# Kernel tuning notes

Measured on AMD Instinct MI355X. Metric: run time of the kernel, lower is better.

The kernel has to match this reference:

```python
import jax, jax.numpy as jnp
import numpy as np

N = 50000        # num nodes
E = 800000       # num edges (before self loops)
IN = 256         # in_channels
H = 4            # heads
C = 32           # out_channels per head
NEG_SLOPE = 0.2


def _glorot(key, shape):
    fan = shape[-2] * (shape[-1] if len(shape) > 2 else 1) + shape[-1]
    # PyG glorot: uniform(-s, s) with s = sqrt(6 / (fan_in + fan_out))
    s = float(np.sqrt(6.0 / (shape[-2] + shape[-1])))
    return jax.random.uniform(key, shape, jnp.float32, -s, s)


def setup_inputs() -> dict:
    key = jax.random.key(0)
    k1, k2, k3, k4, k5 = jax.random.split(key, 5)
    x = jax.random.normal(k1, (N, IN), jnp.float32)
    src = jax.random.randint(k2, (E,), 0, N)
    dst = jax.random.randint(k3, (E,), 0, N)
    # guarantee no self loops (module removes them then re-adds exactly N loops)
    dst = jnp.where(dst == src, (dst + 1) % N, dst)
    edge_index = jnp.stack([src, dst]).astype(jnp.int32)
    weight = _glorot(k4, (IN, H * C))
    att = _glorot(k5, (1, H, 2 * C))
    bias = jnp.zeros((H * C,), jnp.float32)
    return {"x": x, "weight": weight, "att": att, "bias": bias,
            "edge_index": edge_index}


def reference(x, weight, att, bias, edge_index):
    n = x.shape[0]
    # linear projection -> [N, H, C]
    h = (x @ weight).reshape(n, H, C)
    # add self loops (input edge_index has none)
    loops = jnp.arange(n, dtype=edge_index.dtype)
    ei = jnp.concatenate([edge_index, jnp.stack([loops, loops])], axis=1)
    src, dst = ei[0], ei[1]          # flow source_to_target: j=src(row 0), i=dst(row 1)
    x_j = h[src]                     # [E', H, C] source features
    x_i = h[dst]                     # [E', H, C] target features
    wl = att[:, :, :C]               # applied to x_i (first half of concat)
    wr = att[:, :, C:]               # applied to x_j
    alpha = (x_i * wl).sum(-1) + (x_j * wr).sum(-1)   # [E', H]
    alpha = jax.nn.leaky_relu(alpha, NEG_SLOPE)
    # NOTE: module normalizes softmax over edge_index[0] (src) segments
    seg = src
    amax = jax.ops.segment_max(alpha, seg, num_segments=n)
    alpha = jnp.exp(alpha - amax[seg])
    denom = jax.ops.segment_sum(alpha, seg, num_segments=n)
    alpha = alpha / (denom[seg] + 1e-16)
    # weighted messages, aggregated at edge_index[i] = edge_index[1] (dst)
    msg = x_j * alpha[:, :, None]                     # [E', H, C]
    out = jax.ops.segment_sum(msg, dst, num_segments=n)  # [N, H, C]
    return out.reshape(n, H * C) + bias
```

## Files before the change

### kernel.cpp

```cpp
#include <hip/hip_runtime.h>
#include <hip/hip_fp16.h>
#include <math.h>


#define NH 4
#define CH 32
#define HC 128
#define IND 256
#define NEG_SLOPE 0.2f
#define CSH 8
#define NCB_MAX 256
#define CHUNK 4096
#define BCAP 6144

typedef __attribute__((ext_vector_type(8))) short bf16x8;
typedef __attribute__((ext_vector_type(16))) float f32x16;

__device__ __forceinline__ unsigned short f2bf(float f) {
    unsigned int u = __float_as_uint(f);
    unsigned int r = (u + 0x7FFFu + ((u >> 16) & 1u)) >> 16;
    return (unsigned short)r;
}
__device__ __forceinline__ float bf2f(unsigned short s) {
    return __uint_as_float(((unsigned int)s) << 16);
}

__global__ __launch_bounds__(256) void k_wprep(const float* __restrict__ W,
                                               unsigned short* __restrict__ WT_bf,
                                               int* __restrict__ gcurS,
                                               int* __restrict__ gcurD) {
    int t = blockIdx.x * 256 + threadIdx.x;
    if (blockIdx.x == 0) { gcurS[threadIdx.x] = 0; gcurD[threadIdx.x] = 0; }
    if (t < IND * HC) {
        int c = t >> 8;
        int k = t & 255;
        WT_bf[t] = f2bf(W[k * HC + c]);
    }
}

__global__ __launch_bounds__(512) void k_gs(const float* __restrict__ x,
                                            const unsigned short* __restrict__ WT_bf,
                                            const float* __restrict__ att,
                                            unsigned short* __restrict__ h_bf,
                                            float* __restrict__ al,
                                            float* __restrict__ ar,
                                            const int* __restrict__ ei,
                                            int* __restrict__ gcurS,
                                            int* __restrict__ gcurD,
                                            unsigned int* __restrict__ recS,
                                            unsigned int* __restrict__ recD,
                                            int E, int NE, int ncb, int ngb, int N) {
    __shared__ __align__(16) unsigned short smem[67840];

    const int tid = threadIdx.x;

    if (blockIdx.x >= ngb) {
        unsigned int* srt = (unsigned int*)smem;
        int* cnt  = (int*)(srt + CHUNK);
        int* off  = cnt + NCB_MAX;
        int* cur  = off + NCB_MAX;
        int* gpos = cur + NCB_MAX;
        int* sc   = gpos + NCB_MAX;

        const int t0 = (blockIdx.x - ngb) * CHUNK;
        const int m  = min(CHUNK, NE - t0);

        unsigned int myrec[CHUNK / 512];
        int nmy = 0;
        for (int i = tid; i < m; i += 512) {
            int t = t0 + i;
            int src, dst;
            if (t < E) { src = ei[t]; dst = ei[E + t]; }
            else       { src = dst = t - E; }
            myrec[nmy++] = (unsigned int)src | ((unsigned int)dst << 16);
        }

        for (int side = 0; side < 2; side++) {
            if (tid < 256) cnt[tid] = 0;
            __syncthreads();
            int mybkt[CHUNK / 512];
            for (int k = 0; k < nmy; k++) {
                unsigned int r = myrec[k];
                int node = side ? (int)(r >> 16) : (int)(r & 0xFFFFu);
                mybkt[k] = node >> CSH;
                atomicAdd(&cnt[mybkt[k]], 1);
            }
            __syncthreads();
            int v = (tid < 256) ? cnt[tid] : 0;
            if (tid < 256) sc[tid] = v;
            __syncthreads();
            for (int o = 1; o < 256; o <<= 1) {
                int t = (tid >= o && tid < 256) ? sc[tid - o] : 0;
                __syncthreads();
                if (tid < 256) sc[tid] += t;
                __syncthreads();
            }
            if (tid < 256) { off[tid] = sc[tid] - v; cur[tid] = sc[tid] - v; }
            __syncthreads();
            for (int k = 0; k < nmy; k++) {
                int p = atomicAdd(&cur[mybkt[k]], 1);
                srt[p] = myrec[k];
            }
            __syncthreads();
            int* gcur = side ? gcurD : gcurS;
            if (tid < ncb) {
                int c = cnt[tid];
                gpos[tid] = c ? atomicAdd(&gcur[tid], c) : 0;
            }
            __syncthreads();
            unsigned int* recX = side ? recD : recS;
            for (int i = tid; i < m; i += 512) {
                unsigned int r = srt[i];
                int node = side ? (int)(r >> 16) : (int)(r & 0xFFFFu);
                int cb = node >> CSH;
                int p  = gpos[cb] + (i - off[cb]);
                if (p < BCAP)
                    recX[(size_t)cb * BCAP + p] = r;
            }
            __syncthreads();
        }
        return;
    }

    unsigned short* xs0 = smem;
    unsigned short* xs1 = smem + 17408;
    unsigned short* wsT = smem + 34816;

    const int row0 = blockIdx.x * 256;
    const int wave = tid >> 6;
    const int lane = tid & 63;
    const int n32  = lane & 31;
    const int half = lane >> 5;

    {
        int c  = tid >> 2;
        int kq = (tid & 3) * 64;
        const unsigned short* src = WT_bf + c * IND + kq;
        unsigned short* dst = wsT + c * 258 + kq;
#pragma unroll
        for (int j = 0; j < 64; j += 8)
            *(int4*)(dst + j) = *(const int4*)(src + j);
    }

    float4 v[8];
#define STAGE_LOAD(p)                                                        \
    {                                                                        \
        _Pragma("unroll")                                                    \
        for (int j = 0; j < 8; j++) {                                        \
            int fid = j * 512 + tid;                                         \
            int gr  = row0 + (fid >> 4);                                     \
            float4 t = make_float4(0.f, 0.f, 0.f, 0.f);                      \
            if (gr < N)                                                      \
                t = *(const float4*)(x + (size_t)gr * IND + (p) * 64 +       \
                                     (fid & 15) * 4);                        \
            v[j] = t;                                                        \
        }                                                                    \
    }
#define STAGE_WRITE(buf)                                                     \
    {                                                                        \
        _Pragma("unroll")                                                    \
        for (int j = 0; j < 8; j++) {                                        \
            int fid = j * 512 + tid;                                         \
            int row = fid >> 4;                                              \
            ushort4 o;                                                       \
            o.x = f2bf(v[j].x); o.y = f2bf(v[j].y);                          \
            o.z = f2bf(v[j].z); o.w = f2bf(v[j].w);                          \
            *(ushort4*)((buf) + row * 68 + (fid & 15) * 4) = o;              \
        }                                                                    \
    }

    STAGE_LOAD(0);
    STAGE_WRITE(xs0);
    __syncthreads();

    f32x16 acc[4];
#pragma unroll
    for (int t = 0; t < 4; t++)
#pragma unroll
        for (int r = 0; r < 16; r++) acc[t][r] = 0.0f;

    const int arow = wave * 32 + n32;
#pragma unroll
    for (int p = 0; p < 4; p++) {
        if (p < 3) STAGE_LOAD(p + 1);
        const unsigned short* xb = (p & 1) ? xs1 : xs0;
#pragma unroll
        for (int s = 0; s < 4; s++) {
            bf16x8 a = *(const bf16x8*)(xb + arow * 68 + s * 16 + half * 8);
#pragma unroll
            for (int t = 0; t < 4; t++) {
                bf16x8 b = *(const bf16x8*)(wsT + (t * 32 + n32) * 258 +
                                            p * 64 + s * 16 + half * 8);
                acc[t] = __builtin_amdgcn_mfma_f32_32x32x16_bf16(a, b, acc[t], 0, 0, 0);
            }
        }
        if (p < 3) STAGE_WRITE((p & 1) ? xs0 : xs1);
        __syncthreads();
    }
#undef STAGE_LOAD
#undef STAGE_WRITE

    float* cs = (float*)smem;
    for (int pass = 0; pass < 2; pass++) {
        if ((wave >> 2) == pass) {
            const int lw = wave & 3;
#pragma unroll
            for (int t = 0; t < 4; t++)
#pragma unroll
                for (int r = 0; r < 16; r++) {
                    int rl = lw * 32 + (r & 3) + 8 * (r >> 2) + 4 * half;
                    cs[rl * 132 + t * 33 + n32] = acc[t][r];
                }
        }
        __syncthreads();

        const int rl   = tid >> 2;
        const int hq   = tid & 3;
        const int orow = row0 + pass * 128 + rl;
        if (orow < N) {
            const float* cr = cs + rl * 132 + hq * 33;
            unsigned short* hp = h_bf + (size_t)orow * HC + hq * CH;
#pragma unroll
            for (int c = 0; c < 32; c += 8) {
                ushort4 o0, o1;
                o0.x = f2bf(cr[c]);     o0.y = f2bf(cr[c + 1]);
                o0.z = f2bf(cr[c + 2]); o0.w = f2bf(cr[c + 3]);
                o1.x = f2bf(cr[c + 4]); o1.y = f2bf(cr[c + 5]);
                o1.z = f2bf(cr[c + 6]); o1.w = f2bf(cr[c + 7]);
                *(ushort4*)(hp + c) = o0;
                *(ushort4*)(hp + c + 4) = o1;
            }
            const float* w0 = att + hq * (2 * CH);
            float sl = 0.f, sr = 0.f;
#pragma unroll
            for (int c = 0; c < CH; c++) {
                float v2 = cr[c];
                sl += v2 * w0[c];
                sr += v2 * w0[CH + c];
            }
            al[orow * NH + hq] = sl;
            ar[orow * NH + hq] = sr;
        }
        __syncthreads();
    }
}

__global__ __launch_bounds__(256) void k_bucket(const unsigned int* __restrict__ recS,
                                                const unsigned int* __restrict__ recD,
                                                const int* __restrict__ gcurS,
                                                const int* __restrict__ gcurD,
                                                const float* __restrict__ al,
                                                const float* __restrict__ ar,
                                                unsigned short* __restrict__ adjD,
                                                int* __restrict__ rowB,
                                                int* __restrict__ rowE,
                                                float* __restrict__ arw,
                                                int ncb, int N) {
    __shared__ int cnt[256], cur[256], sc[256];
    __shared__ float lsums[256 * NH];
    __shared__ float lar[256 * NH];
    const int tid = threadIdx.x;

    if (blockIdx.x < ncb) {
        const int cb = blockIdx.x;
        const int b0 = cb * BCAP;
        const int tot_rec = min(gcurD[cb], BCAP);

        cnt[tid] = 0;
        __syncthreads();
        for (int i = tid; i < tot_rec; i += 256) {
            unsigned int r = recD[b0 + i];
            atomicAdd(&cnt[(r >> 16) & 255], 1);
        }
        __syncthreads();
        int v = cnt[tid];
        sc[tid] = v;
        __syncthreads();
        for (int o = 1; o < 256; o <<= 1) {
            int t = (tid >= o) ? sc[tid - o] : 0;
            __syncthreads();
            sc[tid] += t;
            __syncthreads();
        }
        int ex = sc[tid] - v;
        int node_g = (cb << CSH) + tid;
        if (node_g < N) { rowB[node_g] = b0 + ex; rowE[node_g] = b0 + ex + v; }
        cur[tid] = ex;
        __syncthreads();
        for (int i = tid; i < tot_rec; i += 256) {
            unsigned int r = recD[b0 + i];
            int node = (int)(r >> 16) & 255;
            int p = atomicAdd(&cur[node], 1);
            adjD[b0 + p] = (unsigned short)(r & 0xFFFFu);
        }
    } else {
        const int cb = blockIdx.x - ncb;
        const int b0 = cb * BCAP;
        const int b1 = b0 + min(gcurS[cb], BCAP);
        const int node_g = (cb << CSH) + tid;

        float4 arv = make_float4(0.f, 0.f, 0.f, 0.f);
        if (node_g < N) arv = *(const float4*)(ar + (size_t)node_g * NH);
        *(float4*)(lar + tid * NH) = arv;
        *(float4*)(lsums + tid * NH) = make_float4(0.f, 0.f, 0.f, 0.f);
        __syncthreads();

        int i = b0 + tid;
        for (; i + 256 < b1; i += 512) {
            unsigned int r0 = recS[i];
            unsigned int r1 = recS[i + 256];
            int sl0 = (int)(r0 & 255u), dst0 = (int)(r0 >> 16);
            int sl1 = (int)(r1 & 255u), dst1 = (int)(r1 >> 16);
            float4 av0 = *(const float4*)(al + (size_t)dst0 * NH);
            float4 av1 = *(const float4*)(al + (size_t)dst1 * NH);
            const float* w0 = lar + sl0 * NH;
            const float* w1 = lar + sl1 * NH;
            float a0 = av0.x + w0[0], a1 = av0.y + w0[1];
            float a2 = av0.z + w0[2], a3 = av0.w + w0[3];
            float c0 = av1.x + w1[0], c1 = av1.y + w1[1];
            float c2 = av1.z + w1[2], c3 = av1.w + w1[3];
            a0 = (a0 > 0.f) ? a0 : NEG_SLOPE * a0;
            a1 = (a1 > 0.f) ? a1 : NEG_SLOPE * a1;
            a2 = (a2 > 0.f) ? a2 : NEG_SLOPE * a2;
            a3 = (a3 > 0.f) ? a3 : NEG_SLOPE * a3;
            c0 = (c0 > 0.f) ? c0 : NEG_SLOPE * c0;
            c1 = (c1 > 0.f) ? c1 : NEG_SLOPE * c1;
            c2 = (c2 > 0.f) ? c2 : NEG_SLOPE * c2;
            c3 = (c3 > 0.f) ? c3 : NEG_SLOPE * c3;
            float* s0 = lsums + sl0 * NH;
            float* s1 = lsums + sl1 * NH;
            atomicAdd(s0 + 0, __expf(a0));
            atomicAdd(s0 + 1, __expf(a1));
            atomicAdd(s0 + 2, __expf(a2));
            atomicAdd(s0 + 3, __expf(a3));
            atomicAdd(s1 + 0, __expf(c0));
            atomicAdd(s1 + 1, __expf(c1));
            atomicAdd(s1 + 2, __expf(c2));
            atomicAdd(s1 + 3, __expf(c3));
        }
        if (i < b1) {
            unsigned int r = recS[i];
            int slot = (int)(r & 255u);
            int dst  = (int)(r >> 16);
            float4 alv = *(const float4*)(al + (size_t)dst * NH);
            const float* av = lar + slot * NH;
            float a0 = alv.x + av[0], a1 = alv.y + av[1];
            float a2 = alv.z + av[2], a3 = alv.w + av[3];
            a0 = (a0 > 0.f) ? a0 : NEG_SLOPE * a0;
            a1 = (a1 > 0.f) ? a1 : NEG_SLOPE * a1;
            a2 = (a2 > 0.f) ? a2 : NEG_SLOPE * a2;
            a3 = (a3 > 0.f) ? a3 : NEG_SLOPE * a3;
            float* sp = lsums + slot * NH;
            atomicAdd(sp + 0, __expf(a0));
            atomicAdd(sp + 1, __expf(a1));
            atomicAdd(sp + 2, __expf(a2));
            atomicAdd(sp + 3, __expf(a3));
        }
        __syncthreads();

        if (node_g < N) {
            const float* sp = lsums + tid * NH;
            float4 p0 = make_float4(arv.x, 1.0f / (sp[0] + 1e-16f),
                                    arv.y, 1.0f / (sp[1] + 1e-16f));
            float4 p1 = make_float4(arv.z, 1.0f / (sp[2] + 1e-16f),
                                    arv.w, 1.0f / (sp[3] + 1e-16f));
            *(float4*)(arw + (size_t)node_g * 8)     = p0;
            *(float4*)(arw + (size_t)node_g * 8 + 4) = p1;
        }
    }
}

__global__ __launch_bounds__(256) void k_agg(const int* __restrict__ rowB,
                                             const int* __restrict__ rowE,
                                             const unsigned short* __restrict__ adjD,
                                             const float* __restrict__ al,
                                             const float* __restrict__ arw,
                                             const unsigned short* __restrict__ h_bf,
                                             const float* __restrict__ bias,
                                             float* __restrict__ out, int N) {
    const int g = threadIdx.x >> 5;
    const int n = blockIdx.x * 8 + g;
    if (n >= N) return;
    const int l  = threadIdx.x & 31;
    const int c0 = l * 4;
    const int hh = l >> 3;
    const int beg = rowB[n], end = rowE[n];
    const float alv = al[n * NH + hh];

    float a0 = 0.f, a1 = 0.f, a2 = 0.f, a3 = 0.f;

    for (int base = beg; base < end; base += 32) {
        int idx = base + l;
        int av  = (idx < end) ? (int)adjD[idx] : 0;
        int cnt = min(32, end - base);
        int e = 0;
        for (; e + 4 <= cnt; e += 4) {
            int s0 = __shfl(av, e,     32);
            int s1 = __shfl(av, e + 1, 32);
            int s2 = __shfl(av, e + 2, 32);
            int s3 = __shfl(av, e + 3, 32);
            ushort4 u0 = *(const ushort4*)(h_bf + (size_t)s0 * HC + c0);
            ushort4 u1 = *(const ushort4*)(h_bf + (size_t)s1 * HC + c0);
            ushort4 u2 = *(const ushort4*)(h_bf + (size_t)s2 * HC + c0);
            ushort4 u3 = *(const ushort4*)(h_bf + (size_t)s3 * HC + c0);
            float2 p0 = *(const float2*)(arw + (size_t)s0 * 8 + hh * 2);
            float2 p1 = *(const float2*)(arw + (size_t)s1 * 8 + hh * 2);
            float2 p2 = *(const float2*)(arw + (size_t)s2 * 8 + hh * 2);
            float2 p3 = *(const float2*)(arw + (size_t)s3 * 8 + hh * 2);
            float t0 = alv + p0.x; t0 = (t0 > 0.f) ? t0 : NEG_SLOPE * t0;
            float t1 = alv + p1.x; t1 = (t1 > 0.f) ? t1 : NEG_SLOPE * t1;
            float t2 = alv + p2.x; t2 = (t2 > 0.f) ? t2 : NEG_SLOPE * t2;
            float t3 = alv + p3.x; t3 = (t3 > 0.f) ? t3 : NEG_SLOPE * t3;
            float w0 = __expf(t0) * p0.y;
            float w1 = __expf(t1) * p1.y;
            float w2 = __expf(t2) * p2.y;
            float w3 = __expf(t3) * p3.y;
            a0 += bf2f(u0.x) * w0; a1 += bf2f(u0.y) * w0;
            a2 += bf2f(u0.z) * w0; a3 += bf2f(u0.w) * w0;
            a0 += bf2f(u1.x) * w1; a1 += bf2f(u1.y) * w1;
            a2 += bf2f(u1.z) * w1; a3 += bf2f(u1.w) * w1;
            a0 += bf2f(u2.x) * w2; a1 += bf2f(u2.y) * w2;
            a2 += bf2f(u2.z) * w2; a3 += bf2f(u2.w) * w2;
            a0 += bf2f(u3.x) * w3; a1 += bf2f(u3.y) * w3;
            a2 += bf2f(u3.z) * w3; a3 += bf2f(u3.w) * w3;
        }
        for (; e < cnt; e++) {
            int s0 = __shfl(av, e, 32);
            ushort4 u0 = *(const ushort4*)(h_bf + (size_t)s0 * HC + c0);
            float2 p0 = *(const float2*)(arw + (size_t)s0 * 8 + hh * 2);
            float t0 = alv + p0.x; t0 = (t0 > 0.f) ? t0 : NEG_SLOPE * t0;
            float w0 = __expf(t0) * p0.y;
            a0 += bf2f(u0.x) * w0; a1 += bf2f(u0.y) * w0;
            a2 += bf2f(u0.z) * w0; a3 += bf2f(u0.w) * w0;
        }
    }
    float4 b4 = *(const float4*)(bias + c0);
    *(float4*)(out + (size_t)n * HC + c0) =
        make_float4(a0 + b4.x, a1 + b4.y, a2 + b4.z, a3 + b4.w);
}

extern "C" void kernel_launch(void* const* d_in, const int* in_sizes, int n_in,
                              void* d_out, int out_size, void* d_ws, size_t ws_size,
                              hipStream_t stream) {
    const float* x    = (const float*)d_in[0];
    const float* W    = (const float*)d_in[1];
    const float* att  = (const float*)d_in[2];
    const float* bias = (const float*)d_in[3];
    const int*   ei   = (const int*)d_in[4];

    const int N  = in_sizes[0] / IND;
    const int E  = in_sizes[4] / 2;
    const int NE = E + N;
    const int ncb = (N + (1 << CSH) - 1) >> CSH;
    const int nsb = (NE + CHUNK - 1) / CHUNK;
    const int ngb = (N + 255) / 256;
    float* out = (float*)d_out;
    const int nodeTot = N * NH;
    const size_t capTot = (size_t)ncb * BCAP;

    unsigned short* h_bf  = (unsigned short*)d_ws;
    unsigned short* WT_bf = h_bf + (size_t)N * HC;
    float* al   = (float*)(WT_bf + IND * HC);
    float* ar   = al + nodeTot;
    float* arw  = ar + nodeTot;
    unsigned int* recS = (unsigned int*)(arw + (size_t)N * 8);
    unsigned int* recD = recS + capTot;
    unsigned short* adjD = (unsigned short*)(recD + capTot);
    int* rowB    = (int*)(adjD + capTot + (capTot & 1));
    int* rowE    = rowB + N;
    int* gcurS   = rowE + N;
    int* gcurD   = gcurS + NCB_MAX;

    k_wprep<<<(IND * HC + 255) / 256, 256, 0, stream>>>(W, WT_bf, gcurS, gcurD);
    k_gs<<<ngb + nsb, 512, 0, stream>>>(x, WT_bf, att, h_bf, al, ar, ei,
                                        gcurS, gcurD, recS, recD,
                                        E, NE, ncb, ngb, N);
    k_bucket<<<2 * ncb, 256, 0, stream>>>(recS, recD, gcurS, gcurD, al, ar,
                                          adjD, rowB, rowE, arw, ncb, N);
    k_agg<<<(N + 7) / 8, 256, 0, stream>>>(rowB, rowE, adjD, al, arw, h_bf,
                                           bias, out, N);
}
```

Before: 212.9 us.

## Stream weight slices per K-step and shrink GEMM LDS to single buffer

```diff
diff --git a/kernel.cpp b/kernel.cpp
--- a/kernel.cpp
+++ b/kernel.cpp
@@ -49,20 +49,20 @@
                                             int* __restrict__ gcurD,
                                             unsigned int* __restrict__ recS,
                                             unsigned int* __restrict__ recD,
-                                            int E, int NE, int ncb, int ngb, int N) {
-    __shared__ __align__(16) unsigned short smem[67840];
+                                            int E, int NE, int ncb, int nsb, int N) {
+    __shared__ float cs[128 * 132];
 
     const int tid = threadIdx.x;
 
-    if (blockIdx.x >= ngb) {
-        unsigned int* srt = (unsigned int*)smem;
+    if (blockIdx.x < nsb) {
+        unsigned int* srt = (unsigned int*)cs;
         int* cnt  = (int*)(srt + CHUNK);
         int* off  = cnt + NCB_MAX;
         int* cur  = off + NCB_MAX;
         int* gpos = cur + NCB_MAX;
         int* sc   = gpos + NCB_MAX;
 
-        const int t0 = (blockIdx.x - ngb) * CHUNK;
+        const int t0 = blockIdx.x * CHUNK;
         const int m  = min(CHUNK, NE - t0);
 
         unsigned int myrec[CHUNK / 512];
@@ -122,28 +122,19 @@
         return;
     }
 
-    unsigned short* xs0 = smem;
-    unsigned short* xs1 = smem + 17408;
-    unsigned short* wsT = smem + 34816;
-
-    const int row0 = blockIdx.x * 256;
+    unsigned short* xs  = (unsigned short*)cs;
+    unsigned short* wsP = (unsigned short*)cs + 17408;
+
+    const int row0 = (blockIdx.x - nsb) * 256;
     const int wave = tid >> 6;
     const int lane = tid & 63;
     const int n32  = lane & 31;
     const int half = lane >> 5;
 
-    {
-        int c  = tid >> 2;
-        int kq = (tid & 3) * 64;
-        const unsigned short* src = WT_bf + c * IND + kq;
-        unsigned short* dst = wsT + c * 258 + kq;
-#pragma unroll
-        for (int j = 0; j < 64; j += 8)
-            *(int4*)(dst + j) = *(const int4*)(src + j);
-    }
-
-    float4 v[8];
-#define STAGE_LOAD(p)                                                        \
+    float4 xv[8];
+    int4   wv0, wv1;
+
+#define XLOAD(p)                                                             \
     {                                                                        \
         _Pragma("unroll")                                                    \
         for (int j = 0; j < 8; j++) {                                        \
@@ -153,54 +144,67 @@
             if (gr < N)                                                      \
                 t = *(const float4*)(x + (size_t)gr * IND + (p) * 64 +       \
                                      (fid & 15) * 4);                        \
-            v[j] = t;                                                        \
+            xv[j] = t;                                                       \
         }                                                                    \
     }
-#define STAGE_WRITE(buf)                                                     \
+#define WLOAD(p)                                                             \
+    {                                                                        \
+        const unsigned short* wp = WT_bf + (tid >> 2) * IND + (p) * 64 +     \
+                                   (tid & 3) * 16;                           \
+        wv0 = *(const int4*)wp;                                              \
+        wv1 = *(const int4*)(wp + 8);                                        \
+    }
+#define XWRITE()                                                             \
     {                                                                        \
         _Pragma("unroll")                                                    \
         for (int j = 0; j < 8; j++) {                                        \
             int fid = j * 512 + tid;                                         \
             int row = fid >> 4;                                              \
             ushort4 o;                                                       \
-            o.x = f2bf(v[j].x); o.y = f2bf(v[j].y);                          \
-            o.z = f2bf(v[j].z); o.w = f2bf(v[j].w);                          \
-            *(ushort4*)((buf) + row * 68 + (fid & 15) * 4) = o;              \
+            o.x = f2bf(xv[j].x); o.y = f2bf(xv[j].y);                        \
+            o.z = f2bf(xv[j].z); o.w = f2bf(xv[j].w);                        \
+            *(ushort4*)(xs + row * 68 + (fid & 15) * 4) = o;                 \
         }                                                                    \
     }
-
-    STAGE_LOAD(0);
-    STAGE_WRITE(xs0);
+#define WWRITE()                                                             \
+    {                                                                        \
+        unsigned short* wq = wsP + (tid >> 2) * 68 + (tid & 3) * 16;         \
+        *(int4*)wq       = wv0;                                              \
+        *(int4*)(wq + 8) = wv1;                                              \
+    }
+
+    XLOAD(0); WLOAD(0);
+
+    f32x16 acc[4];
+#pragma unroll
+    for (int t = 0; t < 4; t++)
+#pragma unroll
+        for (int r = 0; r < 16; r++) acc[t][r] = 0.0f;
+
+    const int arow = wave * 32 + n32;
+#pragma unroll
+    for (int p = 0; p < 4; p++) {
+        __syncthreads();
+        XWRITE(); WWRITE();
+        __syncthreads();
+        if (p < 3) { XLOAD(p + 1); WLOAD(p + 1); }
+#pragma unroll
+        for (int s = 0; s < 4; s++) {
+            bf16x8 a = *(const bf16x8*)(xs + arow * 68 + s * 16 + half * 8);
+#pragma unroll
+            for (int t = 0; t < 4; t++) {
+                bf16x8 b = *(const bf16x8*)(wsP + (t * 32 + n32) * 68 +
+                                            s * 16 + half * 8);
+                acc[t] = __builtin_amdgcn_mfma_f32_32x32x16_bf16(a, b, acc[t], 0, 0, 0);
+            }
+        }
+    }
+#undef XLOAD
+#undef WLOAD
+#undef XWRITE
+#undef WWRITE
     __syncthreads();
 
-    f32x16 acc[4];
-#pragma unroll
-    for (int t = 0; t < 4; t++)
-#pragma unroll
-        for (int r = 0; r < 16; r++) acc[t][r] = 0.0f;
-
-    const int arow = wave * 32 + n32;
-#pragma unroll
-    for (int p = 0; p < 4; p++) {
-        if (p < 3) STAGE_LOAD(p + 1);
-        const unsigned short* xb = (p & 1) ? xs1 : xs0;
-#pragma unroll
-        for (int s = 0; s < 4; s++) {
-            bf16x8 a = *(const bf16x8*)(xb + arow * 68 + s * 16 + half * 8);
-#pragma unroll
-            for (int t = 0; t < 4; t++) {
-                bf16x8 b = *(const bf16x8*)(wsT + (t * 32 + n32) * 258 +
-                                            p * 64 + s * 16 + half * 8);
-                acc[t] = __builtin_amdgcn_mfma_f32_32x32x16_bf16(a, b, acc[t], 0, 0, 0);
-            }
-        }
-        if (p < 3) STAGE_WRITE((p & 1) ? xs0 : xs1);
-        __syncthreads();
-    }
-#undef STAGE_LOAD
-#undef STAGE_WRITE
-
-    float* cs = (float*)smem;
     for (int pass = 0; pass < 2; pass++) {
         if ((wave >> 2) == pass) {
             const int lw = wave & 3;
@@ -472,9 +476,9 @@
     int* gcurD   = gcurS + NCB_MAX;
 
     k_wprep<<<(IND * HC + 255) / 256, 256, 0, stream>>>(W, WT_bf, gcurS, gcurD);
-    k_gs<<<ngb + nsb, 512, 0, stream>>>(x, WT_bf, att, h_bf, al, ar, ei,
+    k_gs<<<nsb + ngb, 512, 0, stream>>>(x, WT_bf, att, h_bf, al, ar, ei,
                                         gcurS, gcurD, recS, recD,
-                                        E, NE, ncb, ngb, N);
+                                        E, NE, ncb, nsb, N);
     k_bucket<<<2 * ncb, 256, 0, stream>>>(recS, recD, gcurS, gcurD, al, ar,
                                           adjD, rowB, rowE, arw, ncb, N);
     k_agg<<<(N + 7) / 8, 256, 0, stream>>>(rowB, rowE, adjD, al, arw, h_bf,
```

Measured after the change: 211.5 us. About the same (-0.7%).
